# Kernel optimization log

Measured on AMD Instinct MI355X. Metric: run time of the kernel, lower is better.

The kernel has to match this reference:

```python
import jax, jax.numpy as jnp
import numpy as np


def setup_inputs() -> dict:
    key = jax.random.key(0)
    k1, k2 = jax.random.split(key)
    B, d = 4096, 1023
    S = 2 * d + 1  # 2047
    predictions = jax.random.normal(k1, (B, S, 2), dtype=jnp.float32)
    targets = jax.random.normal(k2, (B, S, 2), dtype=jnp.float32)
    return {"predictions": predictions, "targets": targets, "d": d, "batch_size": B}


def reference(predictions, targets, d, batch_size):
    # Sum of squared differences over batch, the first 2*d+1 positions,
    # and both (x, y) coordinates; normalized by (2d+1) and batch_size.
    S = 2 * d + 1
    diff = predictions[:batch_size, :S, :2] - targets[:batch_size, :S, :2]
    total = jnp.sum(diff * diff)
    return total / S / batch_size
```

## Files before the change

### kernel.cpp

```cpp
#include <hip/hip_runtime.h>

__global__ __launch_bounds__(256) void ssd_partials(const float4* __restrict__ p,
                                                    const float4* __restrict__ t,
                                                    float* __restrict__ ws,
                                                    int n4) {
    const int tid = threadIdx.x;
    const int stride = gridDim.x * blockDim.x;
    const int stride2 = stride * 2;

    float accA0 = 0.f, accA1 = 0.f, accB0 = 0.f, accB1 = 0.f;

    int i = blockIdx.x * blockDim.x + tid;
    #pragma unroll 1
    for (int k = 0; k < 8; ++k, i += stride2) {
        float4 a0 = p[i];
        float4 b0 = t[i];
        float4 a1 = p[i + stride];
        float4 b1 = t[i + stride];
        float d;
        d = a0.x - b0.x; accA0 += d * d;
        d = a0.y - b0.y; accA1 += d * d;
        d = a0.z - b0.z; accA0 += d * d;
        d = a0.w - b0.w; accA1 += d * d;
        d = a1.x - b1.x; accB0 += d * d;
        d = a1.y - b1.y; accB1 += d * d;
        d = a1.z - b1.z; accB0 += d * d;
        d = a1.w - b1.w; accB1 += d * d;
    }

    float acc = (accA0 + accA1) + (accB0 + accB1);

    #pragma unroll
    for (int off = 32; off > 0; off >>= 1)
        acc += __shfl_down(acc, off, 64);

    __shared__ float wave_sums[4];
    const int lane = tid & 63;
    const int wave = tid >> 6;
    if (lane == 0) wave_sums[wave] = acc;
    __syncthreads();

    if (tid == 0)
        ws[blockIdx.x] = (wave_sums[0] + wave_sums[1]) + (wave_sums[2] + wave_sums[3]);
}

__global__ __launch_bounds__(256) void ssd_finalize(const float* __restrict__ ws,
                                                    float* __restrict__ out,
                                                    float scale) {
    const int tid = threadIdx.x;
    float acc = ws[tid] + ws[tid + 256] + ws[tid + 512] + ws[tid + 768];

    #pragma unroll
    for (int off = 32; off > 0; off >>= 1)
        acc += __shfl_down(acc, off, 64);

    __shared__ float wave_sums[4];
    const int lane = tid & 63;
    const int wave = tid >> 6;
    if (lane == 0) wave_sums[wave] = acc;
    __syncthreads();

    if (tid == 0)
        out[0] = ((wave_sums[0] + wave_sums[1]) + (wave_sums[2] + wave_sums[3])) * scale;
}

extern "C" void kernel_launch(void* const* d_in, const int* in_sizes, int n_in,
                              void* d_out, int out_size, void* d_ws, size_t ws_size,
                              hipStream_t stream) {
    const float* pred = (const float*)d_in[0];
    const float* targ = (const float*)d_in[1];
    float* out = (float*)d_out;
    float* ws = (float*)d_ws;

    const int B = 4096;
    const int S = 2047;
    const float scale = 1.0f / ((float)S * (float)B);
    const int n4 = (B * S * 2) / 4;

    ssd_partials<<<1024, 256, 0, stream>>>((const float4*)pred,
                                           (const float4*)targ,
                                           ws, n4);
    ssd_finalize<<<1, 256, 0, stream>>>(ws, out, scale);
}
```

Measured before the change: 150.0 us.

## Use contiguous per-block chunks with all loads issued up front

Each block now owns a contiguous 2048-float4 chunk, with 2047 blocks instead of 1024 grid-strided blocks. All 16 float4 loads per thread are issued before any arithmetic to raise memory-level parallelism. The finalize kernel is widened to sum 2047 partials. This trades more blocks and higher register pressure for a fully unrolled load phase and a simpler address pattern.

```diff
diff --git a/kernel.cpp b/kernel.cpp
--- a/kernel.cpp
+++ b/kernel.cpp
@@ -1,34 +1,26 @@
 #include <hip/hip_runtime.h>
 
-__global__ __launch_bounds__(256) void ssd_partials(const float4* __restrict__ p,
-                                                    const float4* __restrict__ t,
-                                                    float* __restrict__ ws,
-                                                    int n4) {
+__global__ __launch_bounds__(256, 4) void ssd_partials(const float4* __restrict__ p,
+                                                       const float4* __restrict__ t,
+                                                       float* __restrict__ ws) {
     const int tid = threadIdx.x;
-    const int stride = gridDim.x * blockDim.x;
-    const int stride2 = stride * 2;
+    const long long base = (long long)blockIdx.x * 2048 + tid;
 
-    float accA0 = 0.f, accA1 = 0.f, accB0 = 0.f, accB1 = 0.f;
+    float4 a[8], b[8];
+    #pragma unroll
+    for (int u = 0; u < 8; ++u) a[u] = p[base + u * 256];
+    #pragma unroll
+    for (int u = 0; u < 8; ++u) b[u] = t[base + u * 256];
 
-    int i = blockIdx.x * blockDim.x + tid;
-    #pragma unroll 1
-    for (int k = 0; k < 8; ++k, i += stride2) {
-        float4 a0 = p[i];
-        float4 b0 = t[i];
-        float4 a1 = p[i + stride];
-        float4 b1 = t[i + stride];
-        float d;
-        d = a0.x - b0.x; accA0 += d * d;
-        d = a0.y - b0.y; accA1 += d * d;
-        d = a0.z - b0.z; accA0 += d * d;
-        d = a0.w - b0.w; accA1 += d * d;
-        d = a1.x - b1.x; accB0 += d * d;
-        d = a1.y - b1.y; accB1 += d * d;
-        d = a1.z - b1.z; accB0 += d * d;
-        d = a1.w - b1.w; accB1 += d * d;
+    float acc0 = 0.f, acc1 = 0.f, acc2 = 0.f, acc3 = 0.f;
+    #pragma unroll
+    for (int u = 0; u < 8; ++u) {
+        float dx = a[u].x - b[u].x; acc0 += dx * dx;
+        float dy = a[u].y - b[u].y; acc1 += dy * dy;
+        float dz = a[u].z - b[u].z; acc2 += dz * dz;
+        float dw = a[u].w - b[u].w; acc3 += dw * dw;
     }
-
-    float acc = (accA0 + accA1) + (accB0 + accB1);
+    float acc = (acc0 + acc1) + (acc2 + acc3);
 
     #pragma unroll
     for (int off = 32; off > 0; off >>= 1)
@@ -48,7 +40,12 @@
                                                     float* __restrict__ out,
                                                     float scale) {
     const int tid = threadIdx.x;
-    float acc = ws[tid] + ws[tid + 256] + ws[tid + 512] + ws[tid + 768];
+    float acc = 0.f;
+    #pragma unroll
+    for (int k = 0; k < 8; ++k) {
+        int idx = tid + k * 256;
+        if (idx < 2047) acc += ws[idx];
+    }
 
     #pragma unroll
     for (int off = 32; off > 0; off >>= 1)
@@ -75,10 +72,8 @@
     const int B = 4096;
     const int S = 2047;
     const float scale = 1.0f / ((float)S * (float)B);
-    const int n4 = (B * S * 2) / 4;
 
-    ssd_partials<<<1024, 256, 0, stream>>>((const float4*)pred,
-                                           (const float4*)targ,
-                                           ws, n4);
+    ssd_partials<<<2047, 256, 0, stream>>>((const float4*)pred,
+                                           (const float4*)targ, ws);
     ssd_finalize<<<1, 256, 0, stream>>>(ws, out, scale);
 }
```

Result: faster. 146.5 us (-2.3%).
